# Performance work log

Measured on AMD Instinct MI355X. Metric: run time of the kernel, lower is better.

Reference implementation:

```python
import jax, jax.numpy as jnp
import numpy as np

TOL = 1e-7
DAMP = 0.05  # m <- 0.95*m + 0.05*tanh(h + J@m)


def setup_inputs() -> dict:
    n = 8192
    key = jax.random.key(0)
    k1, k2 = jax.random.split(key)
    h = 0.1 * jax.random.normal(k1, (n,), dtype=jnp.float32)
    J = 0.1 * jax.random.normal(k2, (n, n), dtype=jnp.float32)
    return {"h": h, "J": J, "max_iter": 100}


def reference(h, J, max_iter):
    # symmetrize J and zero the diagonal, as in _symmetrize_J
    Js = (J + J.T) * 0.5
    Js = Js * (1.0 - jnp.eye(Js.shape[0], dtype=Js.dtype))

    def step(carry, _):
        m, done = carry
        m_new = jnp.tanh(h + Js @ m)
        conv = jnp.linalg.norm(m_new - m) < TOL
        # torch breaks BEFORE the damped update when converged -> freeze m
        stop = done | conv
        m_next = jnp.where(stop, m, (1.0 - DAMP) * m + DAMP * m_new)
        return (m_next, stop), None

    m0 = jnp.zeros_like(h)
    (m, _), _ = jax.lax.scan(step, (m0, jnp.array(False)), None, length=max_iter)

    cov = jnp.outer(m, m) + jnp.diag(m * (1.0 - m))
    cov_flat = jnp.triu(cov, k=1).reshape(-1)  # keeps zeros below diag, like torch .triu(1).flatten()
    return m, cov_flat
```

## Files before the change

kernel.cpp:

```cpp
#include <hip/hip_runtime.h>
#include <math.h>

#define N 8192
#define T 128
#define NT 64
#define NTILES 2080
#define NHALF (NTILES*2)
#define TILE_BYTES 40960
#define MAXIT 100
#define DAMP 0.05f
#define QSCALE 1099511627776.0f
#define QINV   9.094947017729282e-13f
#define JQ     1048576.0f
#define JDEQ   9.5367431640625e-7f


__device__ __forceinline__ void decode_tile(int k, int& I, int& Jb) {
  int rem = k, i = 0;
  while (rem >= NT - i) { rem -= NT - i; ++i; }
  I = i; Jb = i + rem;
}

__global__ __launch_bounds__(256) void sympack_kernel(
    const float* __restrict__ J, char* __restrict__ Jp) {
  int blk = blockIdx.x;
  int sub = blk & 3, k = blk >> 2;
  int I, Jb; decode_tile(k, I, Jb);
  int sr = sub >> 1, sc = sub & 1;
  int r0 = I * T + sr * 64;
  int c0 = Jb * T + sc * 64;
  __shared__ float bl[64][65];
  int tid = threadIdx.x;
  #pragma unroll
  for (int it = 0; it < 4; ++it) {
    int s = tid + 256 * it;
    int br = s >> 4, q = s & 15;
    float4 v = *reinterpret_cast<const float4*>(J + (size_t)(c0 + br) * N + r0 + 4 * q);
    bl[br][4 * q + 0] = v.x; bl[br][4 * q + 1] = v.y;
    bl[br][4 * q + 2] = v.z; bl[br][4 * q + 3] = v.w;
  }
  __syncthreads();
  char* tb = Jp + (size_t)k * TILE_BYTES;
  #pragma unroll
  for (int it = 0; it < 4; ++it) {
    int s = tid + 256 * it;
    int r = s >> 4, q = s & 15, c = 4 * q;
    float4 a = *reinterpret_cast<const float4*>(J + (size_t)(r0 + r) * N + c0 + c);
    float4 o;
    o.x = 0.5f * (a.x + bl[c + 0][r]);
    o.y = 0.5f * (a.y + bl[c + 1][r]);
    o.z = 0.5f * (a.z + bl[c + 2][r]);
    o.w = 0.5f * (a.w + bl[c + 3][r]);
    int gi = r0 + r;
    if (gi == c0 + c + 0) o.x = 0.f;
    if (gi == c0 + c + 1) o.y = 0.f;
    if (gi == c0 + c + 2) o.z = 0.f;
    if (gi == c0 + c + 3) o.w = 0.f;
    int q0 = __float2int_rn(fminf(fmaxf(o.x, -0.499999f), 0.499999f) * JQ);
    int q1 = __float2int_rn(fminf(fmaxf(o.y, -0.499999f), 0.499999f) * JQ);
    int q2 = __float2int_rn(fminf(fmaxf(o.z, -0.499999f), 0.499999f) * JQ);
    int q3 = __float2int_rn(fminf(fmaxf(o.w, -0.499999f), 0.499999f) * JQ);
    unsigned int h0 = (unsigned int)(q0 >> 4) & 0xFFFFu, n0 = (unsigned int)q0 & 0xFu;
    unsigned int h1 = (unsigned int)(q1 >> 4) & 0xFFFFu, n1 = (unsigned int)q1 & 0xFu;
    unsigned int h2 = (unsigned int)(q2 >> 4) & 0xFFFFu, n2 = (unsigned int)q2 & 0xFu;
    unsigned int h3 = (unsigned int)(q3 >> 4) & 0xFFFFu, n3 = (unsigned int)q3 & 0xFu;
    size_t eoff = (size_t)(sr * 64 + r) * T + sc * 64 + c;
    *reinterpret_cast<uint2*>(tb + eoff * 2) = make_uint2(h0 | (h1 << 16), h2 | (h3 << 16));
    *reinterpret_cast<unsigned short*>(tb + 32768 + (eoff >> 1)) =
        (unsigned short)(n0 | (n1 << 4) | (n2 << 8) | (n3 << 12));
  }
}

__global__ __launch_bounds__(256, 6) void fused_iter_kernel(
    const char* __restrict__ Jp,
    const unsigned long long* __restrict__ yR,
    unsigned long long* __restrict__ yW,
    unsigned long long* __restrict__ yZ,
    const float* __restrict__ mprev, float* __restrict__ mpub,
    const float* __restrict__ h, int t) {
  int k = blockIdx.x >> 1;
  int qh = blockIdx.x & 1;
  int I, Jb; decode_tile(k, I, Jb);
  const char* tb = Jp + (size_t)k * TILE_BYTES;
  __shared__ float smJ[T], smI[64], rowres[64], colpart[16][T];
  int tid = threadIdx.x;
  int w = tid >> 6, lane = tid & 63;
  int grp = lane >> 4, l16 = lane & 15;

  float4 vhi[4];
  unsigned int vlo[4];
  #pragma unroll
  for (int i = 0; i < 4; ++i) {
    int r = (qh << 6) + (w << 4) + (i << 2) + grp;
    size_t eoff = (size_t)r * T + l16 * 8;
    vhi[i] = *reinterpret_cast<const float4*>(tb + eoff * 2);
    vlo[i] = *reinterpret_cast<const unsigned int*>(tb + 32768 + (eoff >> 1));
  }

  if (tid < 192) {
    int g = (tid < 128) ? (Jb * T + tid) : (I * T + (qh << 6) + (tid - 128));
    float mt;
    if (t == 1) {
      mt = DAMP * tanhf(h[g]);
    } else {
      float y = (float)(long long)yR[g] * QINV;
      mt = fmaf(DAMP, tanhf(h[g] + y), (1.0f - DAMP) * mprev[g]);
    }
    if (I == Jb && tid >= 128) mpub[g] = mt;
    float mts = mt * JDEQ;
    if (tid < 128) smJ[tid] = mts; else smI[tid - 128] = mts;
  }
  __syncthreads();

  float mjs[8];
  #pragma unroll
  for (int e = 0; e < 8; ++e) mjs[e] = smJ[l16 * 8 + e];
  float ca0 = 0.f, ca1 = 0.f, ca2 = 0.f, ca3 = 0.f;
  float ca4 = 0.f, ca5 = 0.f, ca6 = 0.f, ca7 = 0.f;
  #pragma unroll
  for (int i = 0; i < 4; ++i) {
    int rl = (w << 4) + (i << 2) + grp;
    const unsigned int* hu = reinterpret_cast<const unsigned int*>(&vhi[i]);
    unsigned int lx = vlo[i];
    int s0 = (int)(hu[0] << 16) >> 16, s1 = (int)hu[0] >> 16;
    int s2 = (int)(hu[1] << 16) >> 16, s3 = (int)hu[1] >> 16;
    int s4 = (int)(hu[2] << 16) >> 16, s5 = (int)hu[2] >> 16;
    int s6 = (int)(hu[3] << 16) >> 16, s7 = (int)hu[3] >> 16;
    float f0 = (float)(s0 * 16 + (int)(lx & 15u));
    float f1 = (float)(s1 * 16 + (int)((lx >> 4) & 15u));
    float f2 = (float)(s2 * 16 + (int)((lx >> 8) & 15u));
    float f3 = (float)(s3 * 16 + (int)((lx >> 12) & 15u));
    float f4 = (float)(s4 * 16 + (int)((lx >> 16) & 15u));
    float f5 = (float)(s5 * 16 + (int)((lx >> 20) & 15u));
    float f6 = (float)(s6 * 16 + (int)((lx >> 24) & 15u));
    float f7 = (float)(s7 * 16 + (int)(lx >> 28));
    float s = fmaf(f0, mjs[0], fmaf(f1, mjs[1],
              fmaf(f2, mjs[2], fmaf(f3, mjs[3],
              fmaf(f4, mjs[4], fmaf(f5, mjs[5],
              fmaf(f6, mjs[6], f7 * mjs[7])))))));
    #pragma unroll
    for (int off = 1; off < 16; off <<= 1) s += __shfl_xor(s, off);
    if (l16 == 0) rowres[rl] = s;
    float mi = smI[rl];
    ca0 = fmaf(f0, mi, ca0); ca1 = fmaf(f1, mi, ca1);
    ca2 = fmaf(f2, mi, ca2); ca3 = fmaf(f3, mi, ca3);
    ca4 = fmaf(f4, mi, ca4); ca5 = fmaf(f5, mi, ca5);
    ca6 = fmaf(f6, mi, ca6); ca7 = fmaf(f7, mi, ca7);
  }
  {
    int cp = w * 4 + grp, cb = l16 * 8;
    float4* dst = reinterpret_cast<float4*>(&colpart[cp][cb]);
    dst[0] = make_float4(ca0, ca1, ca2, ca3);
    dst[1] = make_float4(ca4, ca5, ca6, ca7);
  }
  __syncthreads();

  if (tid < 64) {
    unsigned long long qr =
        (unsigned long long)(long long)llrintf(rowres[tid] * QSCALE);
    atomicAdd(&yW[I * T + (qh << 6) + tid], qr);
  }
  if (tid < T && Jb != I) {
    float cs = 0.f;
    #pragma unroll
    for (int p = 0; p < 16; ++p) cs += colpart[p][tid];
    unsigned long long qc = (unsigned long long)(long long)llrintf(cs * QSCALE);
    atomicAdd(&yW[Jb * T + tid], qc);
  }

  if (blockIdx.x < 256 && tid < 32) yZ[blockIdx.x * 32 + tid] = 0ull;
}

__global__ __launch_bounds__(256) void finalize_kernel(
    const unsigned long long* __restrict__ yfin, const float* __restrict__ h,
    const float* __restrict__ m99, float* __restrict__ m_out) {
  int g = blockIdx.x * 256 + threadIdx.x;
  float y = (float)(long long)yfin[g] * QINV;
  m_out[g] = fmaf(DAMP, tanhf(h[g] + y), (1.0f - DAMP) * m99[g]);
}

__global__ __launch_bounds__(256) void cov_kernel(
    const float* __restrict__ m, float* __restrict__ cov) {
  size_t qq = (size_t)blockIdx.x * blockDim.x + threadIdx.x;
  size_t idx = qq << 2;
  int i = (int)(idx >> 13);
  int j = (int)(idx & (size_t)(N - 1));
  float mi = m[i];
  float4 mj = *reinterpret_cast<const float4*>(m + j);
  float4 v;
  v.x = (j + 0 > i) ? mi * mj.x : 0.f;
  v.y = (j + 1 > i) ? mi * mj.y : 0.f;
  v.z = (j + 2 > i) ? mi * mj.z : 0.f;
  v.w = (j + 3 > i) ? mi * mj.w : 0.f;
  *reinterpret_cast<float4*>(cov + idx) = v;
}

extern "C" void kernel_launch(void* const* d_in, const int* in_sizes, int n_in,
                              void* d_out, int out_size, void* d_ws, size_t ws_size,
                              hipStream_t stream) {
  const float* h = (const float*)d_in[0];
  const float* J = (const float*)d_in[1];

  float* out = (float*)d_out;
  float* m_arr = out;
  float* base = out + N;
  char* Jp = (char*)base;
  float* mb0 = (float*)(Jp + (size_t)NTILES * TILE_BYTES);
  float* mb1 = mb0 + N;
  unsigned long long* yb = (unsigned long long*)(mb1 + N);

  hipMemsetAsync(yb, 0, 3 * (size_t)N * sizeof(unsigned long long), stream);

  sympack_kernel<<<NTILES * 4, 256, 0, stream>>>(J, Jp);

  for (int t = 1; t < MAXIT; ++t) {
    unsigned long long* yR = yb + (size_t)((t + 2) % 3) * N;
    unsigned long long* yW = yb + (size_t)(t % 3) * N;
    unsigned long long* yZ = yb + (size_t)((t + 1) % 3) * N;
    const float* mprev = (t & 1) ? mb0 : mb1;
    float* mpub = (t & 1) ? mb1 : mb0;
    fused_iter_kernel<<<NHALF, 256, 0, stream>>>(Jp, yR, yW, yZ, mprev, mpub, h, t);
  }
  finalize_kernel<<<N / 256, 256, 0, stream>>>(yb, h, mb1, m_arr);
  cov_kernel<<<(unsigned)(((size_t)N * N / 4) / 256), 256, 0, stream>>>(m_arr, base);
}
```

Baseline: 1.816 ms.

## Process four half-tiles per block with register double-buffered prefetch

```diff
diff --git a/kernel.cpp b/kernel.cpp
--- a/kernel.cpp
+++ b/kernel.cpp
@@ -6,6 +6,8 @@
 #define NT 64
 #define NTILES 2080
 #define NHALF (NTILES*2)
+#define NBLK2 1040
+#define NPASS 4
 #define TILE_BYTES 40960
 #define MAXIT 100
 #define DAMP 0.05f
@@ -71,24 +73,10 @@
   }
 }
 
-__global__ __launch_bounds__(256, 6) void fused_iter_kernel(
-    const char* __restrict__ Jp,
-    const unsigned long long* __restrict__ yR,
-    unsigned long long* __restrict__ yW,
-    unsigned long long* __restrict__ yZ,
-    const float* __restrict__ mprev, float* __restrict__ mpub,
-    const float* __restrict__ h, int t) {
-  int k = blockIdx.x >> 1;
-  int qh = blockIdx.x & 1;
-  int I, Jb; decode_tile(k, I, Jb);
+__device__ __forceinline__ void prefetch_half(
+    const char* __restrict__ Jp, int k, int qh, int w, int grp, int l16,
+    float4 (&vhi)[4], unsigned int (&vlo)[4]) {
   const char* tb = Jp + (size_t)k * TILE_BYTES;
-  __shared__ float smJ[T], smI[64], rowres[64], colpart[16][T];
-  int tid = threadIdx.x;
-  int w = tid >> 6, lane = tid & 63;
-  int grp = lane >> 4, l16 = lane & 15;
-
-  float4 vhi[4];
-  unsigned int vlo[4];
   #pragma unroll
   for (int i = 0; i < 4; ++i) {
     int r = (qh << 6) + (w << 4) + (i << 2) + grp;
@@ -96,7 +84,13 @@
     vhi[i] = *reinterpret_cast<const float4*>(tb + eoff * 2);
     vlo[i] = *reinterpret_cast<const unsigned int*>(tb + 32768 + (eoff >> 1));
   }
-
+}
+
+__device__ __forceinline__ void phase1_m(
+    int I, int Jb, int qh, int tid, int t,
+    const unsigned long long* __restrict__ yR,
+    const float* __restrict__ mprev, float* __restrict__ mpub,
+    const float* __restrict__ h, float* smJ, float* smI) {
   if (tid < 192) {
     int g = (tid < 128) ? (Jb * T + tid) : (I * T + (qh << 6) + (tid - 128));
     float mt;
@@ -110,8 +104,13 @@
     float mts = mt * JDEQ;
     if (tid < 128) smJ[tid] = mts; else smI[tid - 128] = mts;
   }
-  __syncthreads();
-
+}
+
+__device__ __forceinline__ void consume_half(
+    const float4 (&vhi)[4], const unsigned int (&vlo)[4],
+    int I, int Jb, int qh, int tid, int w, int grp, int l16,
+    unsigned long long* __restrict__ yW,
+    const float* smJ, const float* smI, float* rowres, float (*colpart)[T]) {
   float mjs[8];
   #pragma unroll
   for (int e = 0; e < 8; ++e) mjs[e] = smJ[l16 * 8 + e];
@@ -154,7 +153,6 @@
     dst[1] = make_float4(ca4, ca5, ca6, ca7);
   }
   __syncthreads();
-
   if (tid < 64) {
     unsigned long long qr =
         (unsigned long long)(long long)llrintf(rowres[tid] * QSCALE);
@@ -167,8 +165,54 @@
     unsigned long long qc = (unsigned long long)(long long)llrintf(cs * QSCALE);
     atomicAdd(&yW[Jb * T + tid], qc);
   }
-
-  if (blockIdx.x < 256 && tid < 32) yZ[blockIdx.x * 32 + tid] = 0ull;
+}
+
+__global__ __launch_bounds__(256, 5) void fused_iter_kernel(
+    const char* __restrict__ Jp,
+    const unsigned long long* __restrict__ yR,
+    unsigned long long* __restrict__ yW,
+    unsigned long long* __restrict__ yZ,
+    const float* __restrict__ mprev, float* __restrict__ mpub,
+    const float* __restrict__ h, int t) {
+  __shared__ float smJ[T], smI[64], rowres[64], colpart[16][T];
+  int tid = threadIdx.x;
+  int w = tid >> 6, lane = tid & 63;
+  int grp = lane >> 4, l16 = lane & 15;
+  int bid = blockIdx.x;
+
+  int h0 = bid,             k0 = h0 >> 1, q0 = h0 & 1;
+  int h1 = bid + NBLK2,     k1 = h1 >> 1, q1 = h1 & 1;
+  int h2 = bid + 2 * NBLK2, k2 = h2 >> 1, q2 = h2 & 1;
+  int h3 = bid + 3 * NBLK2, k3 = h3 >> 1, q3 = h3 & 1;
+
+  float4 vhiA[4], vhiB[4];
+  unsigned int vloA[4], vloB[4];
+
+  prefetch_half(Jp, k0, q0, w, grp, l16, vhiA, vloA);
+  int I0, J0; decode_tile(k0, I0, J0);
+  phase1_m(I0, J0, q0, tid, t, yR, mprev, mpub, h, smJ, smI);
+  __syncthreads();
+  prefetch_half(Jp, k1, q1, w, grp, l16, vhiB, vloB);
+  consume_half(vhiA, vloA, I0, J0, q0, tid, w, grp, l16, yW, smJ, smI, rowres, colpart);
+
+  int I1, J1; decode_tile(k1, I1, J1);
+  phase1_m(I1, J1, q1, tid, t, yR, mprev, mpub, h, smJ, smI);
+  __syncthreads();
+  prefetch_half(Jp, k2, q2, w, grp, l16, vhiA, vloA);
+  consume_half(vhiB, vloB, I1, J1, q1, tid, w, grp, l16, yW, smJ, smI, rowres, colpart);
+
+  int I2, J2; decode_tile(k2, I2, J2);
+  phase1_m(I2, J2, q2, tid, t, yR, mprev, mpub, h, smJ, smI);
+  __syncthreads();
+  prefetch_half(Jp, k3, q3, w, grp, l16, vhiB, vloB);
+  consume_half(vhiA, vloA, I2, J2, q2, tid, w, grp, l16, yW, smJ, smI, rowres, colpart);
+
+  int I3, J3; decode_tile(k3, I3, J3);
+  phase1_m(I3, J3, q3, tid, t, yR, mprev, mpub, h, smJ, smI);
+  __syncthreads();
+  consume_half(vhiB, vloB, I3, J3, q3, tid, w, grp, l16, yW, smJ, smI, rowres, colpart);
+
+  if (bid < 256 && tid < 32) yZ[bid * 32 + tid] = 0ull;
 }
 
 __global__ __launch_bounds__(256) void finalize_kernel(
@@ -219,7 +263,7 @@
     unsigned long long* yZ = yb + (size_t)((t + 1) % 3) * N;
     const float* mprev = (t & 1) ? mb0 : mb1;
     float* mpub = (t & 1) ? mb1 : mb0;
-    fused_iter_kernel<<<NHALF, 256, 0, stream>>>(Jp, yR, yW, yZ, mprev, mpub, h, t);
+    fused_iter_kernel<<<NBLK2, 256, 0, stream>>>(Jp, yR, yW, yZ, mprev, mpub, h, t);
   }
   finalize_kernel<<<N / 256, 256, 0, stream>>>(yb, h, mb1, m_arr);
   cov_kernel<<<(unsigned)(((size_t)N * N / 4) / 256), 256, 0, stream>>>(m_arr, base);
```

New measurement: 2.316 ms. 1.28x slower.
